# Kernel tuning notes

Hardware: AMD Instinct MI355X
Metric: run time of the kernel (lower is better)

Reference implementation:

```python
import jax, jax.numpy as jnp
import numpy as np

NUM_CODES = 8192
DIM = 256
TAU = 1.0
KL_WEIGHT = 0.01
COMMIT_WEIGHT = 0.25
B, C, P = 8, 64, 32


def setup_inputs() -> dict:
    key = jax.random.key(0)
    kz, kc = jax.random.split(key)
    z = jax.random.normal(kz, (B, C, P, DIM), dtype=jnp.float32)
    # nn.init.normal_(codebook.weight, std=1/sqrt(dim))
    codebook = jax.random.normal(kc, (NUM_CODES, DIM), dtype=jnp.float32) / jnp.sqrt(jnp.float32(DIM))
    return {"z": z, "codebook": codebook}


def reference(z, codebook):
    Bq, Cq, Pq, D = z.shape
    flat = z.reshape(-1, D)                                  # (N, D)
    logits = flat @ codebook.T                               # (N, num_codes)
    # training path: gumbel-softmax (hard=False), fixed key for determinism
    g = jax.random.gumbel(jax.random.key(42), logits.shape, dtype=logits.dtype)
    soft_one_hot = jax.nn.softmax((logits + g) / TAU, axis=-1)
    z_q = (soft_one_hot @ codebook).reshape(Bq, Cq, Pq, D)
    # KL to uniform prior: sum(qy * log(qy * K + 1e-10))
    log_qy = jax.nn.log_softmax(logits, axis=-1)
    qy = jnp.exp(log_qy)
    kl_loss = KL_WEIGHT * jnp.mean(jnp.sum(qy * jnp.log(qy * NUM_CODES + 1e-10), axis=-1))
    codes = jnp.argmax(logits, axis=-1).reshape(Bq, Cq, Pq)
    commit_loss = COMMIT_WEIGHT * jnp.mean((jax.lax.stop_gradient(z_q) - z) ** 2)
    z_q_st = z + jax.lax.stop_gradient(z_q - z)              # straight-through
    total_loss = commit_loss + kl_loss
    return (z_q_st, total_loss, codes)
```

## Files before the change

kernel.cpp:

```cpp
#include <hip/hip_runtime.h>
#include <stdint.h>
#include <math.h>

#define N_ROWS   16384
#define N_CODES  8192
#define DIMV     256
#define RT       32
#define CK       32
#define NCHUNK   (N_CODES / CK)
#define CK2      64
#define NITER    (N_CODES / CK2)
#define OUT_ZQ_N ((size_t)N_ROWS * DIMV)
#define OUT_LOSS OUT_ZQ_N
#define OUT_CODE (OUT_ZQ_N + 1)

#define WS_CBHI 0u
#define WS_CBT  4194304u
#define WS_ACC  8388608u
#define WS_NEED (8388608u + 64u)

#define CBH0_OFF  0
#define CBH1_OFF  33792
#define CBH_SZ    33792
#define BSTRIDE   1056
#define P0_OFF    67584
#define P_BUF_SZ  4608
#define P_ROW     144
#define S2B_OFF   76800
#define SKL_OFF   77312
#define TKL_OFF   77824
#define SMEM_BYTES 78336
#define ZT_ROWF   260
#define CAND_OFF  0

typedef __attribute__((ext_vector_type(8))) short short8;
typedef __attribute__((ext_vector_type(4))) float float4v;

typedef __attribute__((address_space(1))) uint32_t g_u32;
typedef __attribute__((address_space(3))) uint32_t l_u32;

__device__ __forceinline__ void dma16(const void* gsrc, void* ldst) {
  __builtin_amdgcn_global_load_lds((g_u32*)gsrc, (l_u32*)ldst, 16, 0, 0);
}

__device__ __forceinline__ uint32_t rotl32(uint32_t x, int r) {
  return __builtin_rotateleft32(x, (uint32_t)r);
}

__device__ __forceinline__ uint32_t threefry_bits(uint32_t c) {
  const uint32_t k0 = 0u, k1 = 42u;
  const uint32_t k2 = 0x1BD11BDAu ^ k0 ^ k1;
  uint32_t x0 = 0u + k0;
  uint32_t x1 = c + k1;
#define TF_R(r) { x0 += x1; x1 = rotl32(x1, r); x1 ^= x0; }
  TF_R(13) TF_R(15) TF_R(26) TF_R(6)
  x0 += k1; x1 += k2 + 1u;
  TF_R(17) TF_R(29) TF_R(16) TF_R(24)
  x0 += k2; x1 += k0 + 2u;
  TF_R(13) TF_R(15) TF_R(26) TF_R(6)
  x0 += k0; x1 += k1 + 3u;
  TF_R(17) TF_R(29) TF_R(16) TF_R(24)
  x0 += k1; x1 += k2 + 4u;
  TF_R(13) TF_R(15) TF_R(26) TF_R(6)
  x0 += k2; x1 += k0 + 5u;
#undef TF_R
  return x0 ^ x1;
}

__device__ __forceinline__ float gumbel_at_v1(uint32_t idx) {
  uint32_t bits = threefry_bits(idx);
  float u = __uint_as_float((bits >> 9) | 0x3f800000u) - 1.0f;
  u = fmaxf(u, 1.17549435e-38f);
  return -logf(-logf(u));
}

__device__ __forceinline__ unsigned short f2bf(float x) {
  uint32_t u = __float_as_uint(x);
  u += 0x7fffu + ((u >> 16) & 1u);
  return (unsigned short)(u >> 16);
}
__device__ __forceinline__ float bf2f(unsigned short h) {
  return __uint_as_float(((uint32_t)h) << 16);
}

__global__ __launch_bounds__(256)
void vq_prep(const float* __restrict__ cb, char* __restrict__ ws) {
  __shared__ unsigned short lhs[32 * 260];
  const int c = blockIdx.x;
  const int tid = threadIdx.x;
  const int k0 = c * 32;
  unsigned short* cbhi = (unsigned short*)(ws + WS_CBHI);
  unsigned short* cbt  = (unsigned short*)(ws + WS_CBT);
#pragma unroll
  for (int i = 0; i < 8; ++i) {
    int F = tid + i * 256;
    int code = F >> 6, d4 = (F & 63) * 4;
    float4 v = *(const float4*)(cb + (size_t)(k0 + code) * DIMV + d4);
    unsigned short h0 = f2bf(v.x), h1 = f2bf(v.y), h2 = f2bf(v.z), h3 = f2bf(v.w);
    ushort4 hv = {h0, h1, h2, h3};
    *(ushort4*)(cbhi + (size_t)(k0 + code) * DIMV + d4) = hv;
    *(ushort4*)(&lhs[code * 260 + d4]) = hv;
  }
  __syncthreads();
  const int d = tid;
  unsigned short vals[32];
#pragma unroll
  for (int cc = 0; cc < 32; ++cc) vals[cc] = lhs[cc * 260 + d];
  unsigned short* base = cbt + (size_t)c * 8192 + (size_t)d * 32;
#pragma unroll
  for (int j = 0; j < 8; ++j) {
    ushort4 w = {vals[4 * j], vals[4 * j + 1], vals[4 * j + 2], vals[4 * j + 3]};
    *(ushort4*)(base + j * 4) = w;
  }
}

__global__ __launch_bounds__(512, 4)
void vq_main_v5(const float* __restrict__ z, const float* __restrict__ cb,
                float* __restrict__ out, char* __restrict__ ws) {
  __shared__ __align__(16) char sm[SMEM_BYTES];

  if (blockIdx.x & 1) __builtin_amdgcn_s_sleep(80);

  const int tid  = threadIdx.x;
  const int wave = tid >> 6;
  const int lane = tid & 63;
  const int quad = lane >> 4;
  const int n    = lane & 15;
  const int mt   = wave & 1;
  const int nt   = wave >> 1;
  const int r0   = blockIdx.x * RT;
  const int myrow = mt * 16 + quad * 4;
  const char* cbhi_b = ws + WS_CBHI;
  const char* cbt_b  = ws + WS_CBT;
  float* wsA = (float*)(ws + WS_ACC);

  {
    float* zts = (float*)sm;
#pragma unroll
    for (int i = 0; i < 4; ++i) {
      int F = tid + i * 512;
      int row = F >> 6, d4 = (F & 63) * 4;
      *(float4*)(zts + row * ZT_ROWF + d4) =
          *(const float4*)(z + (size_t)(r0 + row) * DIMV + d4);
    }
  }
  __syncthreads();
  short8 zhi[8];
  {
    const float* zts = (const float*)sm;
    const int rowl = mt * 16 + n;
#pragma unroll
    for (int ks = 0; ks < 8; ++ks) {
      const float* zp = zts + rowl * ZT_ROWF + ks * 32 + quad * 8;
      float4 f0 = *(const float4*)zp;
      float4 f1 = *(const float4*)(zp + 4);
      zhi[ks][0] = (short)f2bf(f0.x); zhi[ks][1] = (short)f2bf(f0.y);
      zhi[ks][2] = (short)f2bf(f0.z); zhi[ks][3] = (short)f2bf(f0.w);
      zhi[ks][4] = (short)f2bf(f1.x); zhi[ks][5] = (short)f2bf(f1.y);
      zhi[ks][6] = (short)f2bf(f1.z); zhi[ks][7] = (short)f2bf(f1.w);
    }
  }
  __syncthreads();

#pragma unroll
  for (int i = 0; i < 4; ++i) {
    int b = wave * 4 + i;
    dma16(cbhi_b + (size_t)(2 * b) * 512 + (size_t)lane * 16, sm + CBH0_OFF + b * BSTRIDE);
  }
  __syncthreads();

  float skl[4] = {0.f, 0.f, 0.f, 0.f};
  float tkl[4] = {0.f, 0.f, 0.f, 0.f};
  float s2l[4] = {0.f, 0.f, 0.f, 0.f};
  float v1[4], v2[4];
  int   i1[4], i2[4];
#pragma unroll
  for (int r = 0; r < 4; ++r) {
    v1[r] = -INFINITY; v2[r] = -INFINITY;
    i1[r] = 0x7fffffff; i2[r] = 0x7fffffff;
  }
  const int kc = nt * 16 + n;
  uint32_t idxA = (uint32_t)(r0 + myrow) * (uint32_t)N_CODES + (uint32_t)kc;
  float4v acc2[4];
#pragma unroll
  for (int t = 0; t < 4; ++t) acc2[t] = (float4v){0.f, 0.f, 0.f, 0.f};

  const char* bbase0 = sm + CBH0_OFF + (kc >> 1) * BSTRIDE + (kc & 1) * 512 + quad * 16;
  const char* g2base = cbt_b + ((size_t)(wave * 32 + n) * 32 + (size_t)(quad * 8)) * 2;

  for (int c = 0; c < NITER; ++c) {
    const int par = c & 1;

    const char* bbase = bbase0 + par * CBH_SZ;
    float4v e0 = (float4v){0.f, 0.f, 0.f, 0.f};
    float4v e1 = (float4v){0.f, 0.f, 0.f, 0.f};
#pragma unroll
    for (int ks = 0; ks < 4; ++ks) {
      short8 ba  = *(const short8*)(bbase + (2 * ks) * 64);
      short8 bbv = *(const short8*)(bbase + (2 * ks + 1) * 64);
      e0 = __builtin_amdgcn_mfma_f32_16x16x32_bf16(zhi[2 * ks], ba, e0, 0, 0, 0);
      e1 = __builtin_amdgcn_mfma_f32_16x16x32_bf16(zhi[2 * ks + 1], bbv, e1, 0, 0, 0);
    }
    float4v acc1 = e0 + e1;

    if (c + 1 < NITER) {
      const size_t k1 = (size_t)(c + 1) * CK2;
      char* dst = sm + (par ? CBH0_OFF : CBH1_OFF);
#pragma unroll
      for (int i = 0; i < 4; ++i) {
        int b = wave * 4 + i;
        dma16(cbhi_b + (k1 + 2 * b) * 512 + (size_t)lane * 16, dst + b * BSTRIDE);
      }
    }
    const char* gc = g2base + (size_t)(2 * c) * 16384;
    short8 bb00 = *(const short8*)(gc);
    short8 bb01 = *(const short8*)(gc + 1024);
    short8 bb10 = *(const short8*)(gc + 16384);
    short8 bb11 = *(const short8*)(gc + 16384 + 1024);

    const int codeg0 = c * CK2 + kc;
    char* pw = sm + P0_OFF + par * P_BUF_SZ;
    uint32_t bits4[4];
#pragma unroll
    for (int r = 0; r < 4; ++r)
      bits4[r] = threefry_bits(idxA + (uint32_t)r * (uint32_t)N_CODES);
#pragma unroll
    for (int r = 0; r < 4; ++r) {
      float l = acc1[r];
      uint32_t bits = bits4[r];
      float u = __uint_as_float((bits >> 9) | 0x3f800000u) - 1.0f;
      float t = -0.69314718056f * __log2f(fmaxf(u, 1.17549435e-38f));
      t = fmaxf(t, 1.0e-10f);
      float e = __expf(l);
      skl[r] += e;
      tkl[r] = fmaf(e, l, tkl[r]);
      bool b1 = l > v1[r];
      bool b2 = l > v2[r];
      v2[r] = b1 ? v1[r] : (b2 ? l : v2[r]);
      i2[r] = b1 ? i1[r] : (b2 ? codeg0 : i2[r]);
      v1[r] = b1 ? l : v1[r];
      i1[r] = b1 ? codeg0 : i1[r];
      float p = e * __builtin_amdgcn_rcpf(t) * 6.1442123533282097e-06f;
      unsigned short ph = f2bf(p);
      s2l[r] += bf2f(ph);
      *(unsigned short*)(pw + (myrow + r) * P_ROW + kc * 2) = ph;
    }
    idxA += (uint32_t)CK2;

    __syncthreads();

    {
      const char* pr = sm + P0_OFF + par * P_BUF_SZ;
      short8 pa00 = *(const short8*)(pr + n * P_ROW + quad * 16);
      short8 pa01 = *(const short8*)(pr + n * P_ROW + 64 + quad * 16);
      short8 pa10 = *(const short8*)(pr + (16 + n) * P_ROW + quad * 16);
      short8 pa11 = *(const short8*)(pr + (16 + n) * P_ROW + 64 + quad * 16);
      acc2[0] = __builtin_amdgcn_mfma_f32_16x16x32_bf16(pa00, bb00, acc2[0], 0, 0, 0);
      acc2[0] = __builtin_amdgcn_mfma_f32_16x16x32_bf16(pa01, bb10, acc2[0], 0, 0, 0);
      acc2[1] = __builtin_amdgcn_mfma_f32_16x16x32_bf16(pa00, bb01, acc2[1], 0, 0, 0);
      acc2[1] = __builtin_amdgcn_mfma_f32_16x16x32_bf16(pa01, bb11, acc2[1], 0, 0, 0);
      acc2[2] = __builtin_amdgcn_mfma_f32_16x16x32_bf16(pa10, bb00, acc2[2], 0, 0, 0);
      acc2[2] = __builtin_amdgcn_mfma_f32_16x16x32_bf16(pa11, bb10, acc2[2], 0, 0, 0);
      acc2[3] = __builtin_amdgcn_mfma_f32_16x16x32_bf16(pa10, bb01, acc2[3], 0, 0, 0);
      acc2[3] = __builtin_amdgcn_mfma_f32_16x16x32_bf16(pa11, bb11, acc2[3], 0, 0, 0);
    }
  }

#pragma unroll
  for (int m = 1; m <= 8; m <<= 1) {
#pragma unroll
    for (int r = 0; r < 4; ++r) {
      s2l[r] += __shfl_xor(s2l[r], m);
      skl[r] += __shfl_xor(skl[r], m);
      tkl[r] += __shfl_xor(tkl[r], m);
    }
  }
  if (n == 0) {
    int off = nt * 128 + myrow * 4;
    float4 fs = {s2l[0], s2l[1], s2l[2], s2l[3]};
    *(float4*)(sm + S2B_OFF + off) = fs;
    float4 fk = {skl[0], skl[1], skl[2], skl[3]};
    *(float4*)(sm + SKL_OFF + off) = fk;
    float4 ft = {tkl[0], tkl[1], tkl[2], tkl[3]};
    *(float4*)(sm + TKL_OFF + off) = ft;
  }
#pragma unroll
  for (int r = 0; r < 4; ++r) {
    char* cbase = sm + CAND_OFF + (myrow + r) * 1024 + kc * 16;
    *(float*)(cbase + 0) = v1[r];
    *(int*)(cbase + 4)   = i1[r];
    *(float*)(cbase + 8) = v2[r];
    *(int*)(cbase + 12)  = i2[r];
  }
  __syncthreads();

  if (tid < 32) {
    int r = tid;
    const float* sklb = (const float*)(sm + SKL_OFF);
    const float* tklb = (const float*)(sm + TKL_OFF);
    float S = (sklb[r] + sklb[32 + r]) + (sklb[64 + r] + sklb[96 + r]);
    float T = (tklb[r] + tklb[32 + r]) + (tklb[64 + r] + tklb[96 + r]);
    float klr = T / S - __logf(S) + 9.010913347279288f;
#pragma unroll
    for (int m = 1; m <= 16; m <<= 1) klr += __shfl_xor(klr, m);
    if (r == 0) atomicAdd(&wsA[0], klr);
  }

  if (tid < 64) {
    int r = tid >> 1, h = tid & 1;
    const char* cbase = sm + CAND_OFF + r * 1024 + h * 512;
    float bv[8]; int bi8[8];
#pragma unroll
    for (int k = 0; k < 8; ++k) { bv[k] = -INFINITY; bi8[k] = 0x7fffffff; }
    for (int s = 0; s < 64; ++s) {
      float v = *(const float*)(cbase + s * 8);
      int  id = *(const int*)(cbase + s * 8 + 4);
      if ((v > bv[7]) || (v == bv[7] && id < bi8[7])) {
        float cv = v; int ci = id;
#pragma unroll
        for (int k = 0; k < 8; ++k) {
          bool sw = (cv > bv[k]) || (cv == bv[k] && ci < bi8[k]);
          float tv = bv[k]; int ti = bi8[k];
          if (sw) { bv[k] = cv; bi8[k] = ci; cv = tv; ci = ti; }
        }
      }
    }
    float ovv[8]; int ovi[8];
#pragma unroll
    for (int k = 0; k < 8; ++k) {
      ovv[k] = __shfl_xor(bv[k], 1);
      ovi[k] = __shfl_xor(bi8[k], 1);
    }
#pragma unroll
    for (int kk = 0; kk < 8; ++kk) {
      float cv = ovv[kk]; int ci = ovi[kk];
      if ((cv > bv[7]) || (cv == bv[7] && ci < bi8[7])) {
#pragma unroll
        for (int k = 0; k < 8; ++k) {
          bool sw = (cv > bv[k]) || (cv == bv[k] && ci < bi8[k]);
          float tv = bv[k]; int ti = bi8[k];
          if (sw) { bv[k] = cv; bi8[k] = ci; cv = tv; ci = ti; }
        }
      }
    }
    const float* zp = z + (size_t)(r0 + r) * DIMV;
    double best = -1.0e300;
    int bidx = 0x7fffffff;
#pragma unroll
    for (int k = 0; k < 4; ++k) {
      int cidx = bi8[h * 4 + k];
      const float* cp = cb + (size_t)cidx * DIMV;
      double d = 0.0;
      for (int dd = 0; dd < DIMV; dd += 4) {
        float4 zv = *(const float4*)(zp + dd);
        float4 xv = *(const float4*)(cp + dd);
        d += (double)zv.x * xv.x + (double)zv.y * xv.y +
             (double)zv.z * xv.z + (double)zv.w * xv.w;
      }
      if (d > best || (d == best && cidx < bidx)) { best = d; bidx = cidx; }
    }
    double obest = __shfl_xor(best, 1);
    int    obidx = __shfl_xor(bidx, 1);
    bool take = (obest > best) || (obest == best && obidx < bidx);
    int finali = take ? obidx : bidx;
    if (h == 0) out[OUT_CODE + (size_t)(r0 + r)] = (float)finali;
  }

  float invm0[4], invm1[4];
  {
    const float* s2b = (const float*)(sm + S2B_OFF);
#pragma unroll
    for (int e = 0; e < 4; ++e) {
      int ra = quad * 4 + e, rb = 16 + quad * 4 + e;
      float Sa = (s2b[ra] + s2b[32 + ra]) + (s2b[64 + ra] + s2b[96 + ra]);
      float Sb = (s2b[rb] + s2b[32 + rb]) + (s2b[64 + rb] + s2b[96 + rb]);
      invm0[e] = 1.0f / Sa;
      invm1[e] = 1.0f / Sb;
    }
  }
  float cpart = 0.f;
#pragma unroll
  for (int t = 0; t < 2; ++t) {
    int dim = wave * 32 + t * 16 + n;
#pragma unroll
    for (int ms = 0; ms < 2; ++ms) {
      float4v a = acc2[ms * 2 + t];
#pragma unroll
      for (int e = 0; e < 4; ++e) {
        int row = ms * 16 + quad * 4 + e;
        float q = a[e] * (ms ? invm1[e] : invm0[e]);
        float zv = z[(size_t)(r0 + row) * DIMV + dim];
        float err = q - zv;
        cpart += err * err;
        out[(size_t)(r0 + row) * DIMV + dim] = zv + err;
      }
    }
  }
#pragma unroll
  for (int m = 1; m <= 32; m <<= 1) cpart += __shfl_xor(cpart, m);
  if (lane == 0) atomicAdd(&wsA[1], cpart);
}

#define ZSTRIDE  260
#define CSTRIDE  260
#define PSTRIDE  36
#define RSTRIDE  17

__global__ __launch_bounds__(256, 2)
void vq_main_v1(const float* __restrict__ z, const float* __restrict__ cb,
                float* __restrict__ out, float* __restrict__ ws_acc) {
  __shared__ float zt[RT * ZSTRIDE];
  __shared__ float cbt[CK * CSTRIDE];
  __shared__ float ptile[RT * PSTRIDE];
  __shared__ float redb[RT * RSTRIDE];
  __shared__ float m2s[RT], s2s[RT], scls[RT];

  const int tid = threadIdx.x;
  const int r0  = blockIdx.x * RT;
#pragma unroll
  for (int p = 0; p < 8; ++p) {
    int q = tid + p * 256;
    int i = q >> 6, c4 = (q & 63) * 4;
    *(float4*)(&zt[i * ZSTRIDE + c4]) = *(const float4*)(z + (size_t)(r0 + i) * DIMV + c4);
  }
  if (tid < RT) { m2s[tid] = -INFINITY; s2s[tid] = 0.f; scls[tid] = 0.f; }
  const int tr = tid & 15, tk = tid >> 4, rowg = tid >> 6;
  const int d4 = (tid & 63) * 4;
  float c_m[2][2], c_s[2][2], c_t[2][2];
  int   c_i[2][2];
#pragma unroll
  for (int a = 0; a < 2; ++a)
#pragma unroll
    for (int b = 0; b < 2; ++b) { c_m[a][b] = -INFINITY; c_s[a][b] = 0.f; c_t[a][b] = 0.f; c_i[a][b] = 0; }
  float acc2[8][4];
#pragma unroll
  for (int j = 0; j < 8; ++j)
#pragma unroll
    for (int e = 0; e < 4; ++e) acc2[j][e] = 0.f;
  __syncthreads();
  for (int c = 0; c < NCHUNK; ++c) {
    const int k0 = c * CK;
#pragma unroll
    for (int p = 0; p < 8; ++p) {
      int q = tid + p * 256;
      int i = q >> 6, c4 = (q & 63) * 4;
      *(float4*)(&cbt[i * CSTRIDE + c4]) = *(const float4*)(cb + (size_t)(k0 + i) * DIMV + c4);
    }
    __syncthreads();
    float l00 = 0.f, l01 = 0.f, l10 = 0.f, l11 = 0.f;
    {
      const float* zp0 = &zt[tr * ZSTRIDE];
      const float* zp1 = &zt[(tr + 16) * ZSTRIDE];
      const float* bp0 = &cbt[tk * CSTRIDE];
      const float* bp1 = &cbt[(tk + 16) * CSTRIDE];
#pragma unroll 4
      for (int d = 0; d < DIMV; d += 4) {
        float4 a0 = *(const float4*)(zp0 + d);
        float4 a1 = *(const float4*)(zp1 + d);
        float4 b0 = *(const float4*)(bp0 + d);
        float4 b1 = *(const float4*)(bp1 + d);
        l00 += a0.x*b0.x + a0.y*b0.y + a0.z*b0.z + a0.w*b0.w;
        l01 += a0.x*b1.x + a0.y*b1.y + a0.z*b1.z + a0.w*b1.w;
        l10 += a1.x*b0.x + a1.y*b0.y + a1.z*b0.z + a1.w*b0.w;
        l11 += a1.x*b1.x + a1.y*b1.y + a1.z*b1.z + a1.w*b1.w;
      }
    }
    float lv2[2][2] = {{l00, l01}, {l10, l11}};
    float a2[2][2];
#pragma unroll
    for (int a = 0; a < 2; ++a) {
      int grow = r0 + tr + a * 16;
#pragma unroll
      for (int b = 0; b < 2; ++b) {
        int gk = k0 + tk + b * 16;
        float g  = gumbel_at_v1((uint32_t)grow * (uint32_t)N_CODES + (uint32_t)gk);
        float lv = lv2[a][b];
        a2[a][b] = lv + g;
        if (lv > c_m[a][b]) {
          float sc = expf(c_m[a][b] - lv);
          c_s[a][b] = c_s[a][b] * sc + 1.0f;
          c_t[a][b] = c_t[a][b] * sc + lv;
          c_m[a][b] = lv;
          c_i[a][b] = gk;
        } else {
          float e = expf(lv - c_m[a][b]);
          c_s[a][b] += e;
          c_t[a][b] += e * lv;
        }
      }
    }
    redb[tr * RSTRIDE + tk]        = fmaxf(a2[0][0], a2[0][1]);
    redb[(tr + 16) * RSTRIDE + tk] = fmaxf(a2[1][0], a2[1][1]);
    __syncthreads();
    if (tid < RT) {
      float cm = -INFINITY;
#pragma unroll
      for (int j = 0; j < 16; ++j) cm = fmaxf(cm, redb[tid * RSTRIDE + j]);
      float m2n = fmaxf(m2s[tid], cm);
      scls[tid] = expf(m2s[tid] - m2n);
      m2s[tid]  = m2n;
    }
    __syncthreads();
#pragma unroll
    for (int a = 0; a < 2; ++a) {
      int row = tr + a * 16;
      float m2r = m2s[row];
      float p0 = expf(a2[a][0] - m2r);
      float p1 = expf(a2[a][1] - m2r);
      ptile[row * PSTRIDE + tk]      = p0;
      ptile[row * PSTRIDE + tk + 16] = p1;
      redb[row * RSTRIDE + tk] = p0 + p1;
    }
    __syncthreads();
    if (tid < RT) {
      float ss = 0.f;
#pragma unroll
      for (int j = 0; j < 16; ++j) ss += redb[tid * RSTRIDE + j];
      s2s[tid] = s2s[tid] * scls[tid] + ss;
    }
#pragma unroll
    for (int j = 0; j < 8; ++j) {
      float sc = scls[rowg * 8 + j];
      acc2[j][0] *= sc; acc2[j][1] *= sc; acc2[j][2] *= sc; acc2[j][3] *= sc;
    }
    for (int k4 = 0; k4 < CK; k4 += 4) {
      float4 cb0 = *(const float4*)(&cbt[(k4 + 0) * CSTRIDE + d4]);
      float4 cb1v = *(const float4*)(&cbt[(k4 + 1) * CSTRIDE + d4]);
      float4 cb2 = *(const float4*)(&cbt[(k4 + 2) * CSTRIDE + d4]);
      float4 cb3 = *(const float4*)(&cbt[(k4 + 3) * CSTRIDE + d4]);
#pragma unroll
      for (int j = 0; j < 8; ++j) {
        float4 p4 = *(const float4*)(&ptile[(rowg * 8 + j) * PSTRIDE + k4]);
        acc2[j][0] += p4.x*cb0.x + p4.y*cb1v.x + p4.z*cb2.x + p4.w*cb3.x;
        acc2[j][1] += p4.x*cb0.y + p4.y*cb1v.y + p4.z*cb2.y + p4.w*cb3.y;
        acc2[j][2] += p4.x*cb0.z + p4.y*cb1v.z + p4.z*cb2.z + p4.w*cb3.z;
        acc2[j][3] += p4.x*cb0.w + p4.y*cb1v.w + p4.z*cb2.w + p4.w*cb3.w;
      }
    }
    __syncthreads();
  }
  float* kbuf = cbt;
#pragma unroll
  for (int a = 0; a < 2; ++a) {
    float m0 = c_m[a][0], m1v = c_m[a][1];
    float m, s, t; int bi;
    if (m0 >= m1v) {
      float e = expf(m1v - m0);
      m = m0; s = c_s[a][0] + c_s[a][1] * e; t = c_t[a][0] + c_t[a][1] * e;
    } else {
      float e = expf(m0 - m1v);
      m = m1v; s = c_s[a][0] * e + c_s[a][1]; t = c_t[a][0] * e + c_t[a][1];
    }
    if (m0 > m1v)      bi = c_i[a][0];
    else if (m1v > m0) bi = c_i[a][1];
    else               bi = min(c_i[a][0], c_i[a][1]);
    int row = tr + a * 16;
    kbuf[row * 65 + tk * 4 + 0] = m;
    kbuf[row * 65 + tk * 4 + 1] = s;
    kbuf[row * 65 + tk * 4 + 2] = t;
    kbuf[row * 65 + tk * 4 + 3] = (float)bi;
  }
  __syncthreads();
  if (tid < RT) {
    int r = tid;
    float M = -INFINITY, S = 0.f, T = 0.f, BM = -INFINITY;
    int BI = 0x7fffffff;
    for (int j = 0; j < 16; ++j) {
      float m  = kbuf[r * 65 + j * 4 + 0];
      float s  = kbuf[r * 65 + j * 4 + 1];
      float t  = kbuf[r * 65 + j * 4 + 2];
      int   bi = (int)kbuf[r * 65 + j * 4 + 3];
      if (m <= M) {
        float e = expf(m - M);
        S += s * e; T += t * e;
      } else {
        float e = expf(M - m);
        S = S * e + s; T = T * e + t; M = m;
      }
      if (m > BM || (m == BM && bi < BI)) { BM = m; BI = bi; }
    }
    float kl = logf((float)N_CODES) + T / S - M - logf(S);
    atomicAdd(&ws_acc[0], kl);
    out[OUT_CODE + (size_t)(r0 + r)] = (float)BI;
  }
  float cpart = 0.f;
#pragma unroll
  for (int j = 0; j < 8; ++j) {
    int row  = rowg * 8 + j;
    int grow = r0 + row;
    float inv = 1.0f / s2s[row];
    float4 zv = *(const float4*)(&zt[row * ZSTRIDE + d4]);
    float q0 = acc2[j][0] * inv, q1 = acc2[j][1] * inv;
    float q2 = acc2[j][2] * inv, q3 = acc2[j][3] * inv;
    float e0 = q0 - zv.x, e1 = q1 - zv.y, e2 = q2 - zv.z, e3 = q3 - zv.w;
    cpart += e0*e0 + e1*e1 + e2*e2 + e3*e3;
    float4 o;
    o.x = zv.x + e0; o.y = zv.y + e1; o.z = zv.z + e2; o.w = zv.w + e3;
    *(float4*)(&out[(size_t)grow * DIMV + d4]) = o;
  }
#pragma unroll
  for (int off = 32; off > 0; off >>= 1) cpart += __shfl_down(cpart, off, 64);
  __syncthreads();
  if ((tid & 63) == 0) redb[tid >> 6] = cpart;
  __syncthreads();
  if (tid == 0) {
    float cs = redb[0] + redb[1] + redb[2] + redb[3];
    atomicAdd(&ws_acc[1], cs);
  }
}

__global__ void vq_finalize(const float* __restrict__ ws_acc, float* __restrict__ out) {
  if (threadIdx.x == 0 && blockIdx.x == 0) {
    float kl = 0.01f * (ws_acc[0] / (float)N_ROWS);
    float cm = 0.25f * (ws_acc[1] / (float)OUT_ZQ_N);
    out[OUT_LOSS] = cm + kl;
  }
}

extern "C" void kernel_launch(void* const* d_in, const int* in_sizes, int n_in,
                              void* d_out, int out_size, void* d_ws, size_t ws_size,
                              hipStream_t stream) {
  (void)in_sizes; (void)n_in; (void)out_size;
  const float* z  = (const float*)d_in[0];
  const float* cb = (const float*)d_in[1];
  float* out = (float*)d_out;
  if (ws_size >= (size_t)WS_NEED) {
    char* ws = (char*)d_ws;
    hipMemsetAsync(ws + WS_ACC, 0, 8, stream);
    vq_prep<<<256, 256, 0, stream>>>(cb, ws);
    vq_main_v5<<<N_ROWS / RT, 512, 0, stream>>>(z, cb, out, ws);
    vq_finalize<<<1, 64, 0, stream>>>((const float*)(ws + WS_ACC), out);
  } else {
    float* ws = (float*)d_ws;
    hipMemsetAsync(ws, 0, 8, stream);
    vq_main_v1<<<N_ROWS / RT, 256, 0, stream>>>(z, cb, out, ws);
    vq_finalize<<<1, 64, 0, stream>>>(ws, out);
  }
}
```

Measured before the change: 639.9 us.

## Load codebook MFMA operands directly from global into registers instead of LDS DMA

Drops the double-buffered global_load_lds staging of the bf16 codebook tile and loads each lane's MFMA B-operand fragments straight from global memory into registers, prefetching the next chunk one iteration ahead. This removes LDS traffic, the LDS read instructions and about 34KB of shared memory per block, which may allow higher occupancy. In exchange every wave now reads the codebook from global or L2 on its own, with no sharing through LDS, and the prefetched fragments add register pressure.

```diff
diff --git a/kernel.cpp b/kernel.cpp
--- a/kernel.cpp
+++ b/kernel.cpp
@@ -19,29 +19,19 @@
 #define WS_ACC  8388608u
 #define WS_NEED (8388608u + 64u)
 
-#define CBH0_OFF  0
-#define CBH1_OFF  33792
-#define CBH_SZ    33792
-#define BSTRIDE   1056
-#define P0_OFF    67584
+#define ZC_OFF    0
+#define P0_OFF    33792
 #define P_BUF_SZ  4608
 #define P_ROW     144
-#define S2B_OFF   76800
-#define SKL_OFF   77312
-#define TKL_OFF   77824
-#define SMEM_BYTES 78336
+#define S2B_OFF   43008
+#define SKL_OFF   43520
+#define TKL_OFF   44032
+#define SMEM_BYTES 44544
 #define ZT_ROWF   260
 #define CAND_OFF  0
 
 typedef __attribute__((ext_vector_type(8))) short short8;
 typedef __attribute__((ext_vector_type(4))) float float4v;
-
-typedef __attribute__((address_space(1))) uint32_t g_u32;
-typedef __attribute__((address_space(3))) uint32_t l_u32;
-
-__device__ __forceinline__ void dma16(const void* gsrc, void* ldst) {
-  __builtin_amdgcn_global_load_lds((g_u32*)gsrc, (l_u32*)ldst, 16, 0, 0);
-}
 
 __device__ __forceinline__ uint32_t rotl32(uint32_t x, int r) {
   return __builtin_rotateleft32(x, (uint32_t)r);
@@ -115,7 +105,7 @@
 }
 
 __global__ __launch_bounds__(512, 4)
-void vq_main_v5(const float* __restrict__ z, const float* __restrict__ cb,
+void vq_main_v7(const float* __restrict__ z, const float* __restrict__ cb,
                 float* __restrict__ out, char* __restrict__ ws) {
   __shared__ __align__(16) char sm[SMEM_BYTES];
 
@@ -135,7 +125,7 @@
   float* wsA = (float*)(ws + WS_ACC);
 
   {
-    float* zts = (float*)sm;
+    float* zts = (float*)(sm + ZC_OFF);
 #pragma unroll
     for (int i = 0; i < 4; ++i) {
       int F = tid + i * 512;
@@ -147,7 +137,7 @@
   __syncthreads();
   short8 zhi[8];
   {
-    const float* zts = (const float*)sm;
+    const float* zts = (const float*)(sm + ZC_OFF);
     const int rowl = mt * 16 + n;
 #pragma unroll
     for (int ks = 0; ks < 8; ++ks) {
@@ -162,13 +152,6 @@
   }
   __syncthreads();
 
-#pragma unroll
-  for (int i = 0; i < 4; ++i) {
-    int b = wave * 4 + i;
-    dma16(cbhi_b + (size_t)(2 * b) * 512 + (size_t)lane * 16, sm + CBH0_OFF + b * BSTRIDE);
-  }
-  __syncthreads();
-
   float skl[4] = {0.f, 0.f, 0.f, 0.f};
   float tkl[4] = {0.f, 0.f, 0.f, 0.f};
   float s2l[4] = {0.f, 0.f, 0.f, 0.f};
@@ -185,33 +168,33 @@
 #pragma unroll
   for (int t = 0; t < 4; ++t) acc2[t] = (float4v){0.f, 0.f, 0.f, 0.f};
 
-  const char* bbase0 = sm + CBH0_OFF + (kc >> 1) * BSTRIDE + (kc & 1) * 512 + quad * 16;
+  const char* g1base = cbhi_b + (size_t)kc * 512 + (size_t)(quad * 16);
   const char* g2base = cbt_b + ((size_t)(wave * 32 + n) * 32 + (size_t)(quad * 8)) * 2;
+
+  short8 gf[8];
+#pragma unroll
+  for (int ks = 0; ks < 8; ++ks)
+    gf[ks] = *(const short8*)(g1base + ks * 64);
 
   for (int c = 0; c < NITER; ++c) {
     const int par = c & 1;
 
-    const char* bbase = bbase0 + par * CBH_SZ;
     float4v e0 = (float4v){0.f, 0.f, 0.f, 0.f};
     float4v e1 = (float4v){0.f, 0.f, 0.f, 0.f};
 #pragma unroll
     for (int ks = 0; ks < 4; ++ks) {
-      short8 ba  = *(const short8*)(bbase + (2 * ks) * 64);
-      short8 bbv = *(const short8*)(bbase + (2 * ks + 1) * 64);
-      e0 = __builtin_amdgcn_mfma_f32_16x16x32_bf16(zhi[2 * ks], ba, e0, 0, 0, 0);
-      e1 = __builtin_amdgcn_mfma_f32_16x16x32_bf16(zhi[2 * ks + 1], bbv, e1, 0, 0, 0);
+      e0 = __builtin_amdgcn_mfma_f32_16x16x32_bf16(zhi[2 * ks], gf[2 * ks], e0, 0, 0, 0);
+      e1 = __builtin_amdgcn_mfma_f32_16x16x32_bf16(zhi[2 * ks + 1], gf[2 * ks + 1], e1, 0, 0, 0);
     }
     float4v acc1 = e0 + e1;
 
     if (c + 1 < NITER) {
-      const size_t k1 = (size_t)(c + 1) * CK2;
-      char* dst = sm + (par ? CBH0_OFF : CBH1_OFF);
-#pragma unroll
-      for (int i = 0; i < 4; ++i) {
-        int b = wave * 4 + i;
-        dma16(cbhi_b + (k1 + 2 * b) * 512 + (size_t)lane * 16, dst + b * BSTRIDE);
-      }
-    }
+      const char* gn = g1base + (size_t)(c + 1) * 32768;
+#pragma unroll
+      for (int ks = 0; ks < 8; ++ks)
+        gf[ks] = *(const short8*)(gn + ks * 64);
+    }
+
     const char* gc = g2base + (size_t)(2 * c) * 16384;
     short8 bb00 = *(const short8*)(gc);
     short8 bb01 = *(const short8*)(gc + 1024);
@@ -628,7 +611,7 @@
     char* ws = (char*)d_ws;
     hipMemsetAsync(ws + WS_ACC, 0, 8, stream);
     vq_prep<<<256, 256, 0, stream>>>(cb, ws);
-    vq_main_v5<<<N_ROWS / RT, 512, 0, stream>>>(z, cb, out, ws);
+    vq_main_v7<<<N_ROWS / RT, 512, 0, stream>>>(z, cb, out, ws);
     vq_finalize<<<1, 64, 0, stream>>>((const float*)(ws + WS_ACC), out);
   } else {
     float* ws = (float*)d_ws;
```

Measured after the change: 1.276 ms. 99.4% more time.

## Warp-specialize VQ kernel into logits, softmax, and z_q MFMA wave groups

Applied to the files above, without the earlier changes.

Splits the 8 waves of the fused VQ kernel into specialized roles. Two waves compute the logit MFMAs from bf16 z staged in shared memory. Two waves accumulate the z_q product one chunk behind, holding all 256 output dims in 16 accumulators. Four waves do the gumbel/softmax/top-4 tracking through an LDS staging buffer. The code chunk shrinks to 32, and a packed 64-bit key top-4 replaces the top-2 compare. The aim is to overlap the MFMA, transcendental and RNG work across waves, but it adds an extra barrier per iteration, uses more registers (launch bounds occupancy lowered from 4 to 2), and leaves the MFMA waves idle while the softmax waves work.

```diff
diff --git a/kernel.cpp b/kernel.cpp
--- a/kernel.cpp
+++ b/kernel.cpp
@@ -8,8 +8,8 @@
 #define RT       32
 #define CK       32
 #define NCHUNK   (N_CODES / CK)
-#define CK2      64
-#define NITER    (N_CODES / CK2)
+#define CK3      32
+#define NIT3     (N_CODES / CK3)
 #define OUT_ZQ_N ((size_t)N_ROWS * DIMV)
 #define OUT_LOSS OUT_ZQ_N
 #define OUT_CODE (OUT_ZQ_N + 1)
@@ -19,19 +19,22 @@
 #define WS_ACC  8388608u
 #define WS_NEED (8388608u + 64u)
 
-#define CBH0_OFF  0
+#define ZT_OFF    0
+#define ZT_ROW    264
+#define CBH0_OFF  16896
 #define CBH1_OFF  33792
-#define CBH_SZ    33792
+#define CBH_SZ    16896
 #define BSTRIDE   1056
-#define P0_OFF    67584
-#define P_BUF_SZ  4608
-#define P_ROW     144
-#define S2B_OFF   76800
-#define SKL_OFF   77312
-#define TKL_OFF   77824
-#define SMEM_BYTES 78336
-#define ZT_ROWF   260
-#define CAND_OFF  0
+#define ACC_OFF   50688
+#define ACC_ROW   144
+#define P0_OFF    55296
+#define P_ROW     80
+#define P_BUF_SZ  2560
+#define S2B_OFF   60416
+#define SKL_OFF   60928
+#define TKL_OFF   61440
+#define SMEM_BYTES 61952
+#define CAND_OFF  16896
 
 typedef __attribute__((ext_vector_type(8))) short short8;
 typedef __attribute__((ext_vector_type(4))) float float4v;
@@ -83,6 +86,15 @@
   return __uint_as_float(((uint32_t)h) << 16);
 }
 
+__device__ __forceinline__ uint32_t fkey(float x) {
+  uint32_t b = __float_as_uint(x);
+  return (b & 0x80000000u) ? ~b : (b | 0x80000000u);
+}
+__device__ __forceinline__ float fkey_inv(uint32_t k) {
+  uint32_t b = (k & 0x80000000u) ? (k ^ 0x80000000u) : ~k;
+  return __uint_as_float(b);
+}
+
 __global__ __launch_bounds__(256)
 void vq_prep(const float* __restrict__ cb, char* __restrict__ ws) {
   __shared__ unsigned short lhs[32 * 260];
@@ -114,9 +126,9 @@
   }
 }
 
-__global__ __launch_bounds__(512, 4)
-void vq_main_v5(const float* __restrict__ z, const float* __restrict__ cb,
-                float* __restrict__ out, char* __restrict__ ws) {
+__global__ __launch_bounds__(512, 2)
+void vq_main_v11(const float* __restrict__ z, const float* __restrict__ cb,
+                 float* __restrict__ out, char* __restrict__ ws) {
   __shared__ __align__(16) char sm[SMEM_BYTES];
 
   if (blockIdx.x & 1) __builtin_amdgcn_s_sleep(80);
@@ -126,171 +138,162 @@
   const int lane = tid & 63;
   const int quad = lane >> 4;
   const int n    = lane & 15;
-  const int mt   = wave & 1;
-  const int nt   = wave >> 1;
   const int r0   = blockIdx.x * RT;
-  const int myrow = mt * 16 + quad * 4;
   const char* cbhi_b = ws + WS_CBHI;
   const char* cbt_b  = ws + WS_CBT;
   float* wsA = (float*)(ws + WS_ACC);
 
+  const bool isG1 = (wave < 2);
+  const bool isG2 = (wave == 2 || wave == 3);
+  const int  gw   = wave;
+  const int  g2   = wave - 2;
+  const int  cw   = wave - 4;
+  const int  crow = (quad & 1) * 16 + n;
+  const int  cq   = cw * 2 + (quad >> 1);
+
   {
-    float* zts = (float*)sm;
+    unsigned short* zt = (unsigned short*)(sm + ZT_OFF);
 #pragma unroll
     for (int i = 0; i < 4; ++i) {
       int F = tid + i * 512;
       int row = F >> 6, d4 = (F & 63) * 4;
-      *(float4*)(zts + row * ZT_ROWF + d4) =
-          *(const float4*)(z + (size_t)(r0 + row) * DIMV + d4);
-    }
-  }
-  __syncthreads();
-  short8 zhi[8];
-  {
-    const float* zts = (const float*)sm;
-    const int rowl = mt * 16 + n;
-#pragma unroll
-    for (int ks = 0; ks < 8; ++ks) {
-      const float* zp = zts + rowl * ZT_ROWF + ks * 32 + quad * 8;
-      float4 f0 = *(const float4*)zp;
-      float4 f1 = *(const float4*)(zp + 4);
-      zhi[ks][0] = (short)f2bf(f0.x); zhi[ks][1] = (short)f2bf(f0.y);
-      zhi[ks][2] = (short)f2bf(f0.z); zhi[ks][3] = (short)f2bf(f0.w);
-      zhi[ks][4] = (short)f2bf(f1.x); zhi[ks][5] = (short)f2bf(f1.y);
-      zhi[ks][6] = (short)f2bf(f1.z); zhi[ks][7] = (short)f2bf(f1.w);
-    }
-  }
-  __syncthreads();
-
-#pragma unroll
-  for (int i = 0; i < 4; ++i) {
-    int b = wave * 4 + i;
+      float4 v = *(const float4*)(z + (size_t)(r0 + row) * DIMV + d4);
+      ushort4 hv = {f2bf(v.x), f2bf(v.y), f2bf(v.z), f2bf(v.w)};
+      *(ushort4*)(&zt[row * ZT_ROW + d4]) = hv;
+    }
+  }
+  __syncthreads();
+#pragma unroll
+  for (int i = 0; i < 2; ++i) {
+    int b = wave * 2 + i;
     dma16(cbhi_b + (size_t)(2 * b) * 512 + (size_t)lane * 16, sm + CBH0_OFF + b * BSTRIDE);
   }
   __syncthreads();
 
-  float skl[4] = {0.f, 0.f, 0.f, 0.f};
-  float tkl[4] = {0.f, 0.f, 0.f, 0.f};
-  float s2l[4] = {0.f, 0.f, 0.f, 0.f};
-  float v1[4], v2[4];
-  int   i1[4], i2[4];
-#pragma unroll
-  for (int r = 0; r < 4; ++r) {
-    v1[r] = -INFINITY; v2[r] = -INFINITY;
-    i1[r] = 0x7fffffff; i2[r] = 0x7fffffff;
-  }
-  const int kc = nt * 16 + n;
-  uint32_t idxA = (uint32_t)(r0 + myrow) * (uint32_t)N_CODES + (uint32_t)kc;
-  float4v acc2[4];
-#pragma unroll
-  for (int t = 0; t < 4; ++t) acc2[t] = (float4v){0.f, 0.f, 0.f, 0.f};
-
-  const char* bbase0 = sm + CBH0_OFF + (kc >> 1) * BSTRIDE + (kc & 1) * 512 + quad * 16;
-  const char* g2base = cbt_b + ((size_t)(wave * 32 + n) * 32 + (size_t)(quad * 8)) * 2;
-
-  for (int c = 0; c < NITER; ++c) {
+  float4v acc2[16];
+#pragma unroll
+  for (int t = 0; t < 16; ++t) acc2[t] = (float4v){0.f, 0.f, 0.f, 0.f};
+  uint64_t K0 = 0, K1 = 0, K2 = 0, K3 = 0;
+  float skl = 0.f, tkl = 0.f, s2l = 0.f;
+  uint32_t bits4[4];
+  uint32_t idxA = (uint32_t)(r0 + crow) * (uint32_t)N_CODES + (uint32_t)(cq * 4);
+
+  const char* abase = sm + ZT_OFF + (size_t)(gw * 16 + n) * (ZT_ROW * 2) + quad * 16;
+
+#define G2_BODY(cm, pbuf)                                                        \
+  {                                                                              \
+    const char* pr = sm + P0_OFF + (pbuf) * P_BUF_SZ;                            \
+    short8 pa0 = *(const short8*)(pr + n * P_ROW + quad * 16);                   \
+    short8 pa1 = *(const short8*)(pr + (16 + n) * P_ROW + quad * 16);            \
+    const char* gcb = cbt_b + (size_t)(cm) * 16384 +                             \
+                      (size_t)(g2 * 128 + n) * 64 + (size_t)(quad * 16);         \
+    _Pragma("unroll")                                                            \
+    for (int t = 0; t < 8; ++t) {                                                \
+      short8 bbv = *(const short8*)(gcb + t * 1024);                             \
+      acc2[t * 2 + 0] = __builtin_amdgcn_mfma_f32_16x16x32_bf16(pa0, bbv, acc2[t * 2 + 0], 0, 0, 0); \
+      acc2[t * 2 + 1] = __builtin_amdgcn_mfma_f32_16x16x32_bf16(pa1, bbv, acc2[t * 2 + 1], 0, 0, 0); \
+    }                                                                            \
+  }
+
+  for (int c = 0; c < NIT3; ++c) {
     const int par = c & 1;
 
-    const char* bbase = bbase0 + par * CBH_SZ;
-    float4v e0 = (float4v){0.f, 0.f, 0.f, 0.f};
-    float4v e1 = (float4v){0.f, 0.f, 0.f, 0.f};
-#pragma unroll
-    for (int ks = 0; ks < 4; ++ks) {
-      short8 ba  = *(const short8*)(bbase + (2 * ks) * 64);
-      short8 bbv = *(const short8*)(bbase + (2 * ks + 1) * 64);
-      e0 = __builtin_amdgcn_mfma_f32_16x16x32_bf16(zhi[2 * ks], ba, e0, 0, 0, 0);
-      e1 = __builtin_amdgcn_mfma_f32_16x16x32_bf16(zhi[2 * ks + 1], bbv, e1, 0, 0, 0);
-    }
-    float4v acc1 = e0 + e1;
-
-    if (c + 1 < NITER) {
-      const size_t k1 = (size_t)(c + 1) * CK2;
+    if (isG1) {
+      const char* cbhb = sm + (par ? CBH1_OFF : CBH0_OFF);
+#pragma unroll
+      for (int nt2 = 0; nt2 < 2; ++nt2) {
+        const int kc = nt2 * 16 + n;
+        const char* bbase = cbhb + (kc >> 1) * BSTRIDE + (kc & 1) * 512 + quad * 16;
+        float4v e0 = (float4v){0.f, 0.f, 0.f, 0.f};
+        float4v e1 = (float4v){0.f, 0.f, 0.f, 0.f};
+#pragma unroll
+        for (int ks = 0; ks < 4; ++ks) {
+          short8 za  = *(const short8*)(abase + (2 * ks) * 64);
+          short8 zb8 = *(const short8*)(abase + (2 * ks + 1) * 64);
+          short8 ba  = *(const short8*)(bbase + (2 * ks) * 64);
+          short8 bb2 = *(const short8*)(bbase + (2 * ks + 1) * 64);
+          e0 = __builtin_amdgcn_mfma_f32_16x16x32_bf16(za, ba, e0, 0, 0, 0);
+          e1 = __builtin_amdgcn_mfma_f32_16x16x32_bf16(zb8, bb2, e1, 0, 0, 0);
+        }
+        float4v a1 = e0 + e1;
+        float4 st = {a1[0], a1[1], a1[2], a1[3]};
+        *(float4*)(sm + ACC_OFF + (size_t)(nt2 * 16 + n) * ACC_ROW
+                   + (size_t)((gw * 16 + quad * 4) * 4)) = st;
+      }
+    } else if (isG2) {
+      if (c > 0) { G2_BODY(c - 1, (c - 1) & 1) }
+    } else {
+#pragma unroll
+      for (int j = 0; j < 4; ++j)
+        bits4[j] = threefry_bits(idxA + (uint32_t)j);
+    }
+    __syncthreads();
+
+    if (c + 1 < NIT3 && wave < 4) {
+      const size_t kb = (size_t)((c + 1) * CK3);
       char* dst = sm + (par ? CBH0_OFF : CBH1_OFF);
 #pragma unroll
       for (int i = 0; i < 4; ++i) {
         int b = wave * 4 + i;
-        dma16(cbhi_b + (k1 + 2 * b) * 512 + (size_t)lane * 16, dst + b * BSTRIDE);
-      }
-    }
-    const char* gc = g2base + (size_t)(2 * c) * 16384;
-    short8 bb00 = *(const short8*)(gc);
-    short8 bb01 = *(const short8*)(gc + 1024);
-    short8 bb10 = *(const short8*)(gc + 16384);
-    short8 bb11 = *(const short8*)(gc + 16384 + 1024);
-
-    const int codeg0 = c * CK2 + kc;
-    char* pw = sm + P0_OFF + par * P_BUF_SZ;
-    uint32_t bits4[4];
-#pragma unroll
-    for (int r = 0; r < 4; ++r)
-      bits4[r] = threefry_bits(idxA + (uint32_t)r * (uint32_t)N_CODES);
-#pragma unroll
-    for (int r = 0; r < 4; ++r) {
-      float l = acc1[r];
-      uint32_t bits = bits4[r];
-      float u = __uint_as_float((bits >> 9) | 0x3f800000u) - 1.0f;
-      float t = -0.69314718056f * __log2f(fmaxf(u, 1.17549435e-38f));
-      t = fmaxf(t, 1.0e-10f);
-      float e = __expf(l);
-      skl[r] += e;
-      tkl[r] = fmaf(e, l, tkl[r]);
-      bool b1 = l > v1[r];
-      bool b2 = l > v2[r];
-      v2[r] = b1 ? v1[r] : (b2 ? l : v2[r]);
-      i2[r] = b1 ? i1[r] : (b2 ? codeg0 : i2[r]);
-      v1[r] = b1 ? l : v1[r];
-      i1[r] = b1 ? codeg0 : i1[r];
-      float p = e * __builtin_amdgcn_rcpf(t) * 6.1442123533282097e-06f;
-      unsigned short ph = f2bf(p);
-      s2l[r] += bf2f(ph);
-      *(unsigned short*)(pw + (myrow + r) * P_ROW + kc * 2) = ph;
-    }
-    idxA += (uint32_t)CK2;
-
+        dma16(cbhi_b + (kb + 2 * b) * 512 + (size_t)lane * 16, dst + b * BSTRIDE);
+      }
+    }
+    if (wave >= 4) {
+      const char* accp = sm + ACC_OFF;
+      float lv[4];
+#pragma unroll
+      for (int j = 0; j < 4; ++j)
+        lv[j] = *(const float*)(accp + (size_t)(cq * 4 + j) * ACC_ROW + (size_t)(crow * 4));
+      char* pw = sm + P0_OFF + par * P_BUF_SZ;
+      unsigned short ph4[4];
+#pragma unroll
+      for (int j = 0; j < 4; ++j) {
+        float l = lv[j];
+        uint32_t bits = bits4[j];
+        float u = __uint_as_float((bits >> 9) | 0x3f800000u) - 1.0f;
+        float t = -0.69314718056f * __log2f(fmaxf(u, 1.17549435e-38f));
+        t = fmaxf(t, 1.0e-10f);
+        float e = __expf(l);
+        skl += e;
+        tkl = fmaf(e, l, tkl);
+        int cg = c * CK3 + cq * 4 + j;
+        uint64_t key = ((uint64_t)fkey(l) << 32) | (uint32_t)(~(uint32_t)cg);
+        bool b1 = key > K0, b2 = key > K1, b3 = key > K2, b4 = key > K3;
+        K3 = b3 ? K2 : (b4 ? key : K3);
+        K2 = b2 ? K1 : (b3 ? key : K2);
+        K1 = b1 ? K0 : (b2 ? key : K1);
+        K0 = b1 ? key : K0;
+        float p = e * __builtin_amdgcn_rcpf(t) * 6.1442123533282097e-06f;
+        ph4[j] = f2bf(p);
+        s2l += bf2f(ph4[j]);
+      }
+      ushort4 pv = {ph4[0], ph4[1], ph4[2], ph4[3]};
+      *(ushort4*)(pw + crow * P_ROW + cq * 8) = pv;
+      idxA += (uint32_t)CK3;
+    }
     __syncthreads();
-
-    {
-      const char* pr = sm + P0_OFF + par * P_BUF_SZ;
-      short8 pa00 = *(const short8*)(pr + n * P_ROW + quad * 16);
-      short8 pa01 = *(const short8*)(pr + n * P_ROW + 64 + quad * 16);
-      short8 pa10 = *(const short8*)(pr + (16 + n) * P_ROW + quad * 16);
-      short8 pa11 = *(const short8*)(pr + (16 + n) * P_ROW + 64 + quad * 16);
-      acc2[0] = __builtin_amdgcn_mfma_f32_16x16x32_bf16(pa00, bb00, acc2[0], 0, 0, 0);
-      acc2[0] = __builtin_amdgcn_mfma_f32_16x16x32_bf16(pa01, bb10, acc2[0], 0, 0, 0);
-      acc2[1] = __builtin_amdgcn_mfma_f32_16x16x32_bf16(pa00, bb01, acc2[1], 0, 0, 0);
-      acc2[1] = __builtin_amdgcn_mfma_f32_16x16x32_bf16(pa01, bb11, acc2[1], 0, 0, 0);
-      acc2[2] = __builtin_amdgcn_mfma_f32_16x16x32_bf16(pa10, bb00, acc2[2], 0, 0, 0);
-      acc2[2] = __builtin_amdgcn_mfma_f32_16x16x32_bf16(pa11, bb10, acc2[2], 0, 0, 0);
-      acc2[3] = __builtin_amdgcn_mfma_f32_16x16x32_bf16(pa10, bb01, acc2[3], 0, 0, 0);
-      acc2[3] = __builtin_amdgcn_mfma_f32_16x16x32_bf16(pa11, bb11, acc2[3], 0, 0, 0);
-    }
-  }
-
-#pragma unroll
-  for (int m = 1; m <= 8; m <<= 1) {
-#pragma unroll
-    for (int r = 0; r < 4; ++r) {
-      s2l[r] += __shfl_xor(s2l[r], m);
-      skl[r] += __shfl_xor(skl[r], m);
-      tkl[r] += __shfl_xor(tkl[r], m);
-    }
-  }
-  if (n == 0) {
-    int off = nt * 128 + myrow * 4;
-    float4 fs = {s2l[0], s2l[1], s2l[2], s2l[3]};
-    *(float4*)(sm + S2B_OFF + off) = fs;
-    float4 fk = {skl[0], skl[1], skl[2], skl[3]};
-    *(float4*)(sm + SKL_OFF + off) = fk;
-    float4 ft = {tkl[0], tkl[1], tkl[2], tkl[3]};
-    *(float4*)(sm + TKL_OFF + off) = ft;
-  }
-#pragma unroll
-  for (int r = 0; r < 4; ++r) {
-    char* cbase = sm + CAND_OFF + (myrow + r) * 1024 + kc * 16;
-    *(float*)(cbase + 0) = v1[r];
-    *(int*)(cbase + 4)   = i1[r];
-    *(float*)(cbase + 8) = v2[r];
-    *(int*)(cbase + 12)  = i2[r];
+  }
+  if (isG2) { G2_BODY(NIT3 - 1, (NIT3 - 1) & 1) }
+#undef G2_BODY
+
+  if (wave >= 4) {
+    skl += __shfl_xor(skl, 32);
+    tkl += __shfl_xor(tkl, 32);
+    s2l += __shfl_xor(s2l, 32);
+    if (quad < 2) {
+      *(float*)(sm + SKL_OFF + cw * 128 + crow * 4) = skl;
+      *(float*)(sm + TKL_OFF + cw * 128 + crow * 4) = tkl;
+      *(float*)(sm + S2B_OFF + cw * 128 + crow * 4) = s2l;
+    }
+    char* cbase = sm + CAND_OFF + (size_t)crow * 256 + (size_t)cq * 32;
+    uint64_t Ks[4] = {K0, K1, K2, K3};
+#pragma unroll
+    for (int k = 0; k < 4; ++k) {
+      float v = fkey_inv((uint32_t)(Ks[k] >> 32));
+      int idx = (int)(~(uint32_t)Ks[k]);
+      *(float*)(cbase + k * 8) = v;
+      *(int*)(cbase + k * 8 + 4) = idx;
+    }
   }
   __syncthreads();
 
@@ -308,11 +311,11 @@
 
   if (tid < 64) {
     int r = tid >> 1, h = tid & 1;
-    const char* cbase = sm + CAND_OFF + r * 1024 + h * 512;
+    const char* cbase = sm + CAND_OFF + r * 256 + h * 128;
     float bv[8]; int bi8[8];
 #pragma unroll
     for (int k = 0; k < 8; ++k) { bv[k] = -INFINITY; bi8[k] = 0x7fffffff; }
-    for (int s = 0; s < 64; ++s) {
+    for (int s = 0; s < 16; ++s) {
       float v = *(const float*)(cbase + s * 8);
       int  id = *(const int*)(cbase + s * 8 + 4);
       if ((v > bv[7]) || (v == bv[7] && id < bi8[7])) {
@@ -366,39 +369,41 @@
     if (h == 0) out[OUT_CODE + (size_t)(r0 + r)] = (float)finali;
   }
 
-  float invm0[4], invm1[4];
-  {
-    const float* s2b = (const float*)(sm + S2B_OFF);
-#pragma unroll
-    for (int e = 0; e < 4; ++e) {
-      int ra = quad * 4 + e, rb = 16 + quad * 4 + e;
-      float Sa = (s2b[ra] + s2b[32 + ra]) + (s2b[64 + ra] + s2b[96 + ra]);
-      float Sb = (s2b[rb] + s2b[32 + rb]) + (s2b[64 + rb] + s2b[96 + rb]);
-      invm0[e] = 1.0f / Sa;
-      invm1[e] = 1.0f / Sb;
-    }
-  }
-  float cpart = 0.f;
-#pragma unroll
-  for (int t = 0; t < 2; ++t) {
-    int dim = wave * 32 + t * 16 + n;
-#pragma unroll
-    for (int ms = 0; ms < 2; ++ms) {
-      float4v a = acc2[ms * 2 + t];
+  if (isG2) {
+    float invm0[4], invm1[4];
+    {
+      const float* s2b = (const float*)(sm + S2B_OFF);
 #pragma unroll
       for (int e = 0; e < 4; ++e) {
-        int row = ms * 16 + quad * 4 + e;
-        float q = a[e] * (ms ? invm1[e] : invm0[e]);
-        float zv = z[(size_t)(r0 + row) * DIMV + dim];
-        float err = q - zv;
-        cpart += err * err;
-        out[(size_t)(r0 + row) * DIMV + dim] = zv + err;
-      }
-    }
-  }
-#pragma unroll
-  for (int m = 1; m <= 32; m <<= 1) cpart += __shfl_xor(cpart, m);
-  if (lane == 0) atomicAdd(&wsA[1], cpart);
+        int ra = quad * 4 + e, rb = 16 + quad * 4 + e;
+        float Sa = (s2b[ra] + s2b[32 + ra]) + (s2b[64 + ra] + s2b[96 + ra]);
+        float Sb = (s2b[rb] + s2b[32 + rb]) + (s2b[64 + rb] + s2b[96 + rb]);
+        invm0[e] = 1.0f / Sa;
+        invm1[e] = 1.0f / Sb;
+      }
+    }
+    float cpart = 0.f;
+#pragma unroll
+    for (int t = 0; t < 8; ++t) {
+      int dim = g2 * 128 + t * 16 + n;
+#pragma unroll
+      for (int ms = 0; ms < 2; ++ms) {
+        float4v a = acc2[t * 2 + ms];
+#pragma unroll
+        for (int e = 0; e < 4; ++e) {
+          int row = ms * 16 + quad * 4 + e;
+          float q = a[e] * (ms ? invm1[e] : invm0[e]);
+          float zv = z[(size_t)(r0 + row) * DIMV + dim];
+          float err = q - zv;
+          cpart += err * err;
+          out[(size_t)(r0 + row) * DIMV + dim] = zv + err;
+        }
+      }
+    }
+#pragma unroll
+    for (int m = 1; m <= 32; m <<= 1) cpart += __shfl_xor(cpart, m);
+    if (lane == 0) atomicAdd(&wsA[1], cpart);
+  }
 }
 
 #define ZSTRIDE  260
@@ -628,7 +633,7 @@
     char* ws = (char*)d_ws;
     hipMemsetAsync(ws + WS_ACC, 0, 8, stream);
     vq_prep<<<256, 256, 0, stream>>>(cb, ws);
-    vq_main_v5<<<N_ROWS / RT, 512, 0, stream>>>(z, cb, out, ws);
+    vq_main_v11<<<N_ROWS / RT, 512, 0, stream>>>(z, cb, out, ws);
     vq_finalize<<<1, 64, 0, stream>>>((const float*)(ws + WS_ACC), out);
   } else {
     float* ws = (float*)d_ws;
```

After: 1.058 ms. +65.3%, slower.
